# Kernel tuning notes

Hardware: AMD Instinct MI355X
Metric: run time of the kernel (lower is better)

The kernel has to match this reference:

```python
import jax, jax.numpy as jnp
import numpy as np

VOCAB = 50257  # nn.Embedding num_embeddings (vocab)
H = 128        # hidden_size
L = 20         # num_layers
T = 1024       # seq_len (time-major, batch_first=False)
B = 128        # batch


def setup_inputs() -> dict:
    key = jax.random.key(0)
    ks = jax.random.split(key, 6)
    s = 1.0 / np.sqrt(H)  # PyTorch LSTM init range
    return {
        "x": jax.random.randint(ks[0], (T, B), 0, VOCAB, dtype=jnp.int32),
        "emb": jax.random.normal(ks[1], (VOCAB, H), jnp.float32) * 0.02,
        "W_ih": jax.random.uniform(ks[2], (L, 4 * H, H), jnp.float32, -s, s),
        "W_hh": jax.random.uniform(ks[3], (L, 4 * H, H), jnp.float32, -s, s),
        "b_ih": jax.random.uniform(ks[4], (L, 4 * H), jnp.float32, -s, s),
        "b_hh": jax.random.uniform(ks[5], (L, 4 * H), jnp.float32, -s, s),
    }


def _lstm_layer(inp, Wih, Whh, b):
    # inp: [T, B, H]; PyTorch gate order: i, f, g, o
    h0 = jnp.zeros((inp.shape[1], H), inp.dtype)
    c0 = h0

    def step(carry, xt):
        h, c = carry
        pre = xt @ Wih.T + h @ Whh.T + b  # [B, 4H]
        i, f, g, o = jnp.split(pre, 4, axis=-1)
        c = jax.nn.sigmoid(f) * c + jax.nn.sigmoid(i) * jnp.tanh(g)
        h = jax.nn.sigmoid(o) * jnp.tanh(c)
        return (h, c), h

    _, hs = jax.lax.scan(step, (h0, c0), inp)
    return hs  # [T, B, H]


def reference(x, emb, W_ih, W_hh, b_ih, b_hh):
    embedded = emb[x]  # [T, B, H] embedding lookup
    out = embedded
    for l in range(L):  # stacked layers (structural loop, not a data dim)
        out = _lstm_layer(out, W_ih[l], W_hh[l], b_ih[l] + b_hh[l])
    return (out, embedded)
```

## Files before the change

kernel.cpp:

```cpp
#include <hip/hip_runtime.h>

#define T_ 1024
#define B_ 128
#define H_ 128
#define L_ 20
#define G4H_ 512
#define NCH 8
#define RING 64
#define GRP 4
#define FSTRIDE 32

typedef _Float16 f16x8 __attribute__((ext_vector_type(8)));
typedef _Float16 f16x4 __attribute__((ext_vector_type(4)));
typedef float f32x4 __attribute__((ext_vector_type(4)));

__device__ __forceinline__ float fast_sig(float x) {
  float e = __builtin_amdgcn_exp2f(-1.44269504f * x);
  return __builtin_amdgcn_rcpf(1.0f + e);
}
__device__ __forceinline__ float fast_tanh(float x) {
  float e = __builtin_amdgcn_exp2f(2.88539008f * x);
  return 1.0f - 2.0f * __builtin_amdgcn_rcpf(e + 1.0f);
}

__device__ __forceinline__ int flag_ld(const int* p) {
  int r;
  asm volatile("global_load_dword %0, %1, off sc1\n\ts_waitcnt vmcnt(0)"
               : "=v"(r) : "v"(p) : "memory");
  return r;
}
__device__ __forceinline__ void flag_st(int* p, int v) {
  asm volatile("global_store_dword %0, %1, off sc1" :: "v"(p), "v"(v) : "memory");
}
__device__ __forceinline__ void xld_sc1(f16x4* d, const _Float16* p) {
  asm volatile("global_load_dwordx2 %0, %1, off sc1" : "=&v"(*d) : "v"(p) : "memory");
}
__device__ __forceinline__ void xld_plain(f16x4* d, const _Float16* p) {
  asm volatile("global_load_dwordx2 %0, %1, off" : "=&v"(*d) : "v"(p) : "memory");
}
__device__ __forceinline__ void st32_sc1(_Float16* p, f16x8 a, f16x8 b) {
  asm volatile("global_store_dwordx4 %0, %1, off sc1\n\t"
               "global_store_dwordx4 %0, %2, off offset:16 sc1"
               :: "v"(p), "v"(a), "v"(b) : "memory");
}

__global__ void wconv_kernel(const float* __restrict__ Wih, const float* __restrict__ Whh,
                             _Float16* __restrict__ Wif, _Float16* __restrict__ Whf) {
  int i = blockIdx.x * 256 + threadIdx.x;
  if (i < L_ * G4H_ * H_) {
    Wif[i] = (_Float16)Wih[i];
    Whf[i] = (_Float16)Whh[i];
  }
}

__global__ void emb_kernel(const int* __restrict__ xids, const float* __restrict__ emb,
                           float* __restrict__ out_emb, _Float16* __restrict__ X0) {
  int row = blockIdx.x;
  int d = threadIdx.x;
  int tok = xids[row];
  float v = emb[(size_t)tok * H_ + d];
  out_emb[(size_t)row * H_ + d] = v;
  X0[(size_t)row * H_ + d] = (_Float16)v;
}

__launch_bounds__(512, 2)
__global__ void lstm_persist_kernel(const _Float16* __restrict__ Wif,
                                    const _Float16* __restrict__ Whf,
                                    const float* __restrict__ bih,
                                    const float* __restrict__ bhh,
                                    const _Float16* __restrict__ X0,
                                    _Float16* __restrict__ XR,
                                    float* __restrict__ out_h,
                                    int* __restrict__ rdy) {
  const int l = blockIdx.x >> 3;
  const int chunk = blockIdx.x & 7;
  const int lane = threadIdx.x & 63;
  const int wave = threadIdx.x >> 6;
  const int lr = lane & 15;
  const int lhi = lane >> 4;
  const int k0 = lhi * 8;
  const int ub = wave * 16;
  const int xrow = threadIdx.x >> 5;
  const int xseg = threadIdx.x & 31;

  f16x8 wi[4][4], wh[4][4];
  float bias[4];
  {
    const _Float16* wip = Wif + (size_t)l * G4H_ * H_;
    const _Float16* whp = Whf + (size_t)l * G4H_ * H_;
#pragma unroll
    for (int G = 0; G < 4; ++G) {
      int j = G * 128 + ub + lr;
      bias[G] = bih[l * G4H_ + j] + bhh[l * G4H_ + j];
#pragma unroll
      for (int kt = 0; kt < 4; ++kt) {
        wi[G][kt] = *(const f16x8*)(wip + (size_t)j * H_ + kt * 32 + k0);
        wh[G][kt] = *(const f16x8*)(whp + (size_t)j * H_ + kt * 32 + k0);
      }
    }
  }

  float cst[4] = {0.f, 0.f, 0.f, 0.f};
  f16x8 hf[4], xf[4];

  __shared__ _Float16 hstage[GRP][16][136];
  __shared__ _Float16 xstage[2][16][136];

  const size_t tile16 = (size_t)16 * H_;
  const _Float16* ring_in =
      (l > 0) ? XR + (size_t)((l - 1) * NCH + chunk) * RING * tile16 : X0;
  _Float16* ring_out = XR + (size_t)(l * NCH + chunk) * RING * tile16;

  int* rin = rdy + ((l - 1) * NCH + chunk) * FSTRIDE;
  int* rout = rdy + (l * NCH + chunk) * FSTRIDE;
  int* rcons = rdy + ((l + 1) * NCH + chunk) * FSTRIDE;

  auto xsrc = [&](int t) -> const _Float16* {
    return (l == 0) ? X0 + ((size_t)t * B_ + chunk * 16 + xrow) * H_ + xseg * 4
                    : ring_in + (size_t)(t & (RING - 1)) * tile16 + (size_t)xrow * H_ + xseg * 4;
  };

  int rin_cache = 0, rcons_cache = 0;

  for (int tg = 0; tg < T_; tg += GRP) {
    if (wave == 0) {
      if (l > 0 && rin_cache < tg + GRP) {
        int v;
        while ((v = flag_ld(rin)) < tg + GRP) __builtin_amdgcn_s_sleep(2);
        rin_cache = v;
      }
      if (l < L_ - 1) {
        int need = tg + 2 * GRP - RING;
        if (need > 0 && rcons_cache < need) {
          int v;
          while ((v = flag_ld(rcons)) < need) __builtin_amdgcn_s_sleep(2);
          rcons_cache = v;
        }
      }
    }
    __syncthreads();

    {
      f16x4 xs;
      const _Float16* sp = xsrc(tg);
      if (l == 0) xld_plain(&xs, sp); else xld_sc1(&xs, sp);
      asm volatile("s_waitcnt vmcnt(0)" ::: "memory");
      *(f16x4*)&xstage[0][xrow][xseg * 4] = xs;
    }
    asm volatile("s_waitcnt lgkmcnt(0)" ::: "memory");
    __builtin_amdgcn_s_barrier();

#pragma unroll
    for (int ti = 0; ti < GRP; ++ti) {
      const int t = tg + ti;

      if (t > 0) {
        const int ps = (ti + GRP - 1) & (GRP - 1);
#pragma unroll
        for (int kt = 0; kt < 4; ++kt)
          hf[kt] = *(const f16x8*)&hstage[ps][lr][kt * 32 + k0];
      } else {
#pragma unroll
        for (int kt = 0; kt < 4; ++kt)
#pragma unroll
          for (int i = 0; i < 8; ++i) hf[kt][i] = (_Float16)0.0f;
      }
#pragma unroll
      for (int kt = 0; kt < 4; ++kt)
        xf[kt] = *(const f16x8*)&xstage[t & 1][lr][kt * 32 + k0];

      f32x4 ai[4], ah[4];
#pragma unroll
      for (int G = 0; G < 4; ++G) {
        float bv = bias[G];
        ai[G][0] = bv; ai[G][1] = bv; ai[G][2] = bv; ai[G][3] = bv;
        ah[G][0] = 0.f; ah[G][1] = 0.f; ah[G][2] = 0.f; ah[G][3] = 0.f;
      }
#pragma unroll
      for (int kt = 0; kt < 4; ++kt)
#pragma unroll
        for (int G = 0; G < 4; ++G)
          ai[G] = __builtin_amdgcn_mfma_f32_16x16x32_f16(xf[kt], wi[G][kt], ai[G], 0, 0, 0);

      f16x4 xs;
      const bool pre = (ti + 1 < GRP);
      if (pre) {
        const _Float16* sp = xsrc(t + 1);
        if (l == 0) xld_plain(&xs, sp); else xld_sc1(&xs, sp);
      }

#pragma unroll
      for (int kt = 0; kt < 4; ++kt)
#pragma unroll
        for (int G = 0; G < 4; ++G)
          ah[G] = __builtin_amdgcn_mfma_f32_16x16x32_f16(hf[kt], wh[G][kt], ah[G], 0, 0, 0);

      float hnew[4];
#pragma unroll
      for (int r = 0; r < 4; ++r) {
        float pi = ai[0][r] + ah[0][r];
        float pf = ai[1][r] + ah[1][r];
        float pg = ai[2][r] + ah[2][r];
        float po = ai[3][r] + ah[3][r];
        float iv = fast_sig(pi);
        float fv = fast_sig(pf);
        float gv = fast_tanh(pg);
        float ov = fast_sig(po);
        float c = fv * cst[r] + iv * gv;
        cst[r] = c;
        hnew[r] = ov * fast_tanh(c);
      }

      if (l == L_ - 1) {
#pragma unroll
        for (int r = 0; r < 4; ++r)
          out_h[((size_t)t * B_ + chunk * 16 + lhi * 4 + r) * H_ + ub + lr] = hnew[r];
      }

      if (pre) {
        asm volatile("s_waitcnt vmcnt(0)" ::: "memory");
        *(f16x4*)&xstage[(t + 1) & 1][xrow][xseg * 4] = xs;
      }
#pragma unroll
      for (int r = 0; r < 4; ++r) hstage[ti][lhi * 4 + r][ub + lr] = (_Float16)hnew[r];

      asm volatile("s_waitcnt lgkmcnt(0)" ::: "memory");
      __builtin_amdgcn_s_barrier();
    }

    if (l < L_ - 1) {
      const int tid = threadIdx.x;
      const int ti2 = tid >> 7;
      const int rem = tid & 127;
      const int row = rem >> 3;
      const int seg = rem & 7;
      _Float16* dst = ring_out + (size_t)((tg + ti2) & (RING - 1)) * tile16 +
                      (size_t)row * H_ + seg * 16;
      const f16x8* src = (const f16x8*)&hstage[ti2][row][seg * 16];
      st32_sc1(dst, src[0], src[1]);
    }

    __syncthreads();
    if (threadIdx.x == 0) flag_st(rout, tg + GRP);
  }
}

extern "C" void kernel_launch(void* const* d_in, const int* in_sizes, int n_in,
                              void* d_out, int out_size, void* d_ws, size_t ws_size,
                              hipStream_t stream) {
  const int* xids = (const int*)d_in[0];
  const float* emb = (const float*)d_in[1];
  const float* Wih = (const float*)d_in[2];
  const float* Whh = (const float*)d_in[3];
  const float* bih = (const float*)d_in[4];
  const float* bhh = (const float*)d_in[5];
  float* out = (float*)d_out;
  float* out_h = out;
  float* out_emb = out + (size_t)T_ * B_ * H_;

  char* ws = (char*)d_ws;
  const size_t RDY_BYTES = (size_t)L_ * NCH * FSTRIDE * 4;
  const size_t X0_BYTES = (size_t)T_ * B_ * H_ * 2;
  const size_t XR_BYTES = (size_t)L_ * NCH * RING * 16 * H_ * 2;
  const size_t WF_BYTES = (size_t)L_ * G4H_ * H_ * 2;
  int* rdyp = (int*)ws;
  _Float16* X0 = (_Float16*)(ws + RDY_BYTES);
  _Float16* XR = (_Float16*)(ws + RDY_BYTES + X0_BYTES);
  _Float16* Wif = (_Float16*)(ws + RDY_BYTES + X0_BYTES + XR_BYTES);
  _Float16* Whf = (_Float16*)(ws + RDY_BYTES + X0_BYTES + XR_BYTES + WF_BYTES);

  hipMemsetAsync(rdyp, 0, RDY_BYTES, stream);
  wconv_kernel<<<(L_ * G4H_ * H_ + 255) / 256, 256, 0, stream>>>(Wih, Whh, Wif, Whf);
  emb_kernel<<<T_ * B_, H_, 0, stream>>>(xids, emb, out_emb, X0);

  void* args[] = {(void*)&Wif, (void*)&Whf, (void*)&bih, (void*)&bhh,
                  (void*)&X0,  (void*)&XR,  (void*)&out_h, (void*)&rdyp};
  hipLaunchCooperativeKernel((void*)lstm_persist_kernel, dim3(L_ * NCH), dim3(512),
                             args, 0, stream);
}
```

Before: 1.571 ms.

## Software-pipeline input projection one step ahead and deepen x prefetch ring

Restructures the per-timestep loop so the input-to-hidden MFMA for step t+1 is computed in the current step, off the recurrent critical path. The step-t+1 projection is seeded with the bias and accumulated directly with the hidden-state MFMAs, which drops the separate ah accumulators and the add. The x staging buffer grows from two to four slots, with loads issued three steps ahead and the upstream-layer wait target raised to cover the extra lookahead. This costs more registers for the second accumulator set and changes the flag and barrier schedule, including a flag wait before the loop.

New measurement: 1.568 ms. Within noise of the previous version (-0.2%).

```diff
diff --git a/kernel.cpp b/kernel.cpp
--- a/kernel.cpp
+++ b/kernel.cpp
@@ -101,10 +101,14 @@
   }
 
   float cst[4] = {0.f, 0.f, 0.f, 0.f};
-  f16x8 hf[4], xf[4];
+  f16x8 hf[4];
+#pragma unroll
+  for (int kt = 0; kt < 4; ++kt)
+#pragma unroll
+    for (int i = 0; i < 8; ++i) hf[kt][i] = (_Float16)0.0f;
 
   __shared__ _Float16 hstage[GRP][16][136];
-  __shared__ _Float16 xstage[2][16][136];
+  __shared__ _Float16 xstage[4][16][136];
 
   const size_t tile16 = (size_t)16 * H_;
   const _Float16* ring_in =
@@ -122,126 +126,158 @@
 
   int rin_cache = 0, rcons_cache = 0;
 
-  for (int tg = 0; tg < T_; tg += GRP) {
-    if (wave == 0) {
-      if (l > 0 && rin_cache < tg + GRP) {
-        int v;
-        while ((v = flag_ld(rin)) < tg + GRP) __builtin_amdgcn_s_sleep(2);
-        rin_cache = v;
-      }
-      if (l < L_ - 1) {
-        int need = tg + 2 * GRP - RING;
-        if (need > 0 && rcons_cache < need) {
-          int v;
-          while ((v = flag_ld(rcons)) < need) __builtin_amdgcn_s_sleep(2);
-          rcons_cache = v;
+  if (wave == 0 && l > 0) {
+    int tgt = 2 * GRP;
+    int v;
+    while ((v = flag_ld(rin)) < tgt) __builtin_amdgcn_s_sleep(2);
+    rin_cache = v;
+  }
+  __syncthreads();
+  {
+    f16x4 a0, a1, a2;
+    if (l == 0) { xld_plain(&a0, xsrc(0)); xld_plain(&a1, xsrc(1)); xld_plain(&a2, xsrc(2)); }
+    else        { xld_sc1(&a0, xsrc(0));   xld_sc1(&a1, xsrc(1));   xld_sc1(&a2, xsrc(2)); }
+    asm volatile("s_waitcnt vmcnt(0)" ::: "memory");
+    *(f16x4*)&xstage[0][xrow][xseg * 4] = a0;
+    *(f16x4*)&xstage[1][xrow][xseg * 4] = a1;
+    *(f16x4*)&xstage[2][xrow][xseg * 4] = a2;
+  }
+  asm volatile("s_waitcnt lgkmcnt(0)" ::: "memory");
+  __builtin_amdgcn_s_barrier();
+
+  f32x4 ai[4];
+  {
+    f16x8 xf0[4];
+#pragma unroll
+    for (int kt = 0; kt < 4; ++kt) xf0[kt] = *(const f16x8*)&xstage[0][lr][kt * 32 + k0];
+#pragma unroll
+    for (int G = 0; G < 4; ++G) {
+      float bv = bias[G];
+      ai[G][0] = bv; ai[G][1] = bv; ai[G][2] = bv; ai[G][3] = bv;
+    }
+#pragma unroll
+    for (int kt = 0; kt < 4; ++kt)
+#pragma unroll
+      for (int G = 0; G < 4; ++G)
+        ai[G] = __builtin_amdgcn_mfma_f32_16x16x32_f16(xf0[kt], wi[G][kt], ai[G], 0, 0, 0);
+  }
+
+  f16x4 xs;
+  bool xs_pending = false;
+
+  for (int t = 0; t < T_; ++t) {
+    if ((t & (GRP - 1)) == 0 && t > 0) {
+      const int tg = t;
+      if (wave == 0) {
+        if (l > 0) {
+          int tgt = tg + 2 * GRP; if (tgt > T_) tgt = T_;
+          if (rin_cache < tgt) {
+            int v;
+            while ((v = flag_ld(rin)) < tgt) __builtin_amdgcn_s_sleep(2);
+            rin_cache = v;
+          }
+        }
+        if (l < L_ - 1) {
+          int need = tg + 2 * GRP - RING;
+          if (need > 0 && rcons_cache < need) {
+            int v;
+            while ((v = flag_ld(rcons)) < need) __builtin_amdgcn_s_sleep(2);
+            rcons_cache = v;
+          }
         }
       }
-    }
-    __syncthreads();
-
-    {
-      f16x4 xs;
-      const _Float16* sp = xsrc(tg);
+      __builtin_amdgcn_s_barrier();
+    }
+
+    if (t > 0) {
+      const int ps = (t - 1) & (GRP - 1);
+#pragma unroll
+      for (int kt = 0; kt < 4; ++kt)
+        hf[kt] = *(const f16x8*)&hstage[ps][lr][kt * 32 + k0];
+    }
+
+#pragma unroll
+    for (int kt = 0; kt < 4; ++kt)
+#pragma unroll
+      for (int G = 0; G < 4; ++G)
+        ai[G] = __builtin_amdgcn_mfma_f32_16x16x32_f16(hf[kt], wh[G][kt], ai[G], 0, 0, 0);
+
+    const bool have_next = (t + 1 < T_);
+    f32x4 ain[4];
+    if (have_next) {
+      f16x8 xfn[4];
+#pragma unroll
+      for (int kt = 0; kt < 4; ++kt)
+        xfn[kt] = *(const f16x8*)&xstage[(t + 1) & 3][lr][kt * 32 + k0];
+#pragma unroll
+      for (int G = 0; G < 4; ++G) {
+        float bv = bias[G];
+        ain[G][0] = bv; ain[G][1] = bv; ain[G][2] = bv; ain[G][3] = bv;
+      }
+#pragma unroll
+      for (int kt = 0; kt < 4; ++kt)
+#pragma unroll
+        for (int G = 0; G < 4; ++G)
+          ain[G] = __builtin_amdgcn_mfma_f32_16x16x32_f16(xfn[kt], wi[G][kt], ain[G], 0, 0, 0);
+    }
+
+    if (xs_pending) {
+      asm volatile("s_waitcnt vmcnt(0)" ::: "memory");
+      *(f16x4*)&xstage[(t + 2) & 3][xrow][xseg * 4] = xs;
+    }
+    if (t + 3 < T_) {
+      const _Float16* sp = xsrc(t + 3);
       if (l == 0) xld_plain(&xs, sp); else xld_sc1(&xs, sp);
-      asm volatile("s_waitcnt vmcnt(0)" ::: "memory");
-      *(f16x4*)&xstage[0][xrow][xseg * 4] = xs;
-    }
+      xs_pending = true;
+    } else {
+      xs_pending = false;
+    }
+
+    float hnew[4];
+#pragma unroll
+    for (int r = 0; r < 4; ++r) {
+      float iv = fast_sig(ai[0][r]);
+      float fv = fast_sig(ai[1][r]);
+      float gv = fast_tanh(ai[2][r]);
+      float ov = fast_sig(ai[3][r]);
+      float c = fv * cst[r] + iv * gv;
+      cst[r] = c;
+      hnew[r] = ov * fast_tanh(c);
+    }
+
+    if (l == L_ - 1) {
+#pragma unroll
+      for (int r = 0; r < 4; ++r)
+        out_h[((size_t)t * B_ + chunk * 16 + lhi * 4 + r) * H_ + ub + lr] = hnew[r];
+    }
+
+#pragma unroll
+    for (int r = 0; r < 4; ++r) hstage[t & (GRP - 1)][lhi * 4 + r][ub + lr] = (_Float16)hnew[r];
+
+    if (have_next) {
+#pragma unroll
+      for (int G = 0; G < 4; ++G) ai[G] = ain[G];
+    }
+
     asm volatile("s_waitcnt lgkmcnt(0)" ::: "memory");
     __builtin_amdgcn_s_barrier();
 
-#pragma unroll
-    for (int ti = 0; ti < GRP; ++ti) {
-      const int t = tg + ti;
-
-      if (t > 0) {
-        const int ps = (ti + GRP - 1) & (GRP - 1);
-#pragma unroll
-        for (int kt = 0; kt < 4; ++kt)
-          hf[kt] = *(const f16x8*)&hstage[ps][lr][kt * 32 + k0];
-      } else {
-#pragma unroll
-        for (int kt = 0; kt < 4; ++kt)
-#pragma unroll
-          for (int i = 0; i < 8; ++i) hf[kt][i] = (_Float16)0.0f;
+    if ((t & (GRP - 1)) == GRP - 1) {
+      const int tg = t & ~(GRP - 1);
+      if (l < L_ - 1) {
+        const int tid = threadIdx.x;
+        const int ti2 = tid >> 7;
+        const int rem = tid & 127;
+        const int row = rem >> 3;
+        const int seg = rem & 7;
+        _Float16* dst = ring_out + (size_t)((tg + ti2) & (RING - 1)) * tile16 +
+                        (size_t)row * H_ + seg * 16;
+        const f16x8* src = (const f16x8*)&hstage[ti2][row][seg * 16];
+        st32_sc1(dst, src[0], src[1]);
       }
-#pragma unroll
-      for (int kt = 0; kt < 4; ++kt)
-        xf[kt] = *(const f16x8*)&xstage[t & 1][lr][kt * 32 + k0];
-
-      f32x4 ai[4], ah[4];
-#pragma unroll
-      for (int G = 0; G < 4; ++G) {
-        float bv = bias[G];
-        ai[G][0] = bv; ai[G][1] = bv; ai[G][2] = bv; ai[G][3] = bv;
-        ah[G][0] = 0.f; ah[G][1] = 0.f; ah[G][2] = 0.f; ah[G][3] = 0.f;
-      }
-#pragma unroll
-      for (int kt = 0; kt < 4; ++kt)
-#pragma unroll
-        for (int G = 0; G < 4; ++G)
-          ai[G] = __builtin_amdgcn_mfma_f32_16x16x32_f16(xf[kt], wi[G][kt], ai[G], 0, 0, 0);
-
-      f16x4 xs;
-      const bool pre = (ti + 1 < GRP);
-      if (pre) {
-        const _Float16* sp = xsrc(t + 1);
-        if (l == 0) xld_plain(&xs, sp); else xld_sc1(&xs, sp);
-      }
-
-#pragma unroll
-      for (int kt = 0; kt < 4; ++kt)
-#pragma unroll
-        for (int G = 0; G < 4; ++G)
-          ah[G] = __builtin_amdgcn_mfma_f32_16x16x32_f16(hf[kt], wh[G][kt], ah[G], 0, 0, 0);
-
-      float hnew[4];
-#pragma unroll
-      for (int r = 0; r < 4; ++r) {
-        float pi = ai[0][r] + ah[0][r];
-        float pf = ai[1][r] + ah[1][r];
-        float pg = ai[2][r] + ah[2][r];
-        float po = ai[3][r] + ah[3][r];
-        float iv = fast_sig(pi);
-        float fv = fast_sig(pf);
-        float gv = fast_tanh(pg);
-        float ov = fast_sig(po);
-        float c = fv * cst[r] + iv * gv;
-        cst[r] = c;
-        hnew[r] = ov * fast_tanh(c);
-      }
-
-      if (l == L_ - 1) {
-#pragma unroll
-        for (int r = 0; r < 4; ++r)
-          out_h[((size_t)t * B_ + chunk * 16 + lhi * 4 + r) * H_ + ub + lr] = hnew[r];
-      }
-
-      if (pre) {
-        asm volatile("s_waitcnt vmcnt(0)" ::: "memory");
-        *(f16x4*)&xstage[(t + 1) & 1][xrow][xseg * 4] = xs;
-      }
-#pragma unroll
-      for (int r = 0; r < 4; ++r) hstage[ti][lhi * 4 + r][ub + lr] = (_Float16)hnew[r];
-
-      asm volatile("s_waitcnt lgkmcnt(0)" ::: "memory");
-      __builtin_amdgcn_s_barrier();
-    }
-
-    if (l < L_ - 1) {
-      const int tid = threadIdx.x;
-      const int ti2 = tid >> 7;
-      const int rem = tid & 127;
-      const int row = rem >> 3;
-      const int seg = rem & 7;
-      _Float16* dst = ring_out + (size_t)((tg + ti2) & (RING - 1)) * tile16 +
-                      (size_t)row * H_ + seg * 16;
-      const f16x8* src = (const f16x8*)&hstage[ti2][row][seg * 16];
-      st32_sc1(dst, src[0], src[1]);
-    }
-
-    __syncthreads();
-    if (threadIdx.x == 0) flag_st(rout, tg + GRP);
+      __syncthreads();
+      if (threadIdx.x == 0) flag_st(rout, t + 1);
+    }
   }
 }
 
```

## Software-pipeline input projection one step ahead and defer ring stores

Applied to the files above, without the earlier changes.

Restructures the per-timestep loop so the input-projection MFMAs for step t+1 are computed while step t waits on the recurrent path, with ping-pong accumulators. X prefetch now runs four steps ahead into a 4-slot LDS buffer, and vmcnt waits are tuned per slot. The ring write-out and ready-flag publish for a group are deferred to the start of the next group, so their latency overlaps compute. The MFMA operands are swapped so each lane ends up with contiguous 4-wide outputs, which enables vectorized hstage, out_h and bias accesses. The cost is more complex synchronization, where a wrong vmcnt count or flag ordering could cause races.

New measurement: 1.511 ms. -3.9%, faster.

```diff
diff --git a/kernel.cpp b/kernel.cpp
--- a/kernel.cpp
+++ b/kernel.cpp
@@ -9,6 +9,7 @@
 #define RING 64
 #define GRP 4
 #define FSTRIDE 32
+#define STR 136
 
 typedef _Float16 f16x8 __attribute__((ext_vector_type(8)));
 typedef _Float16 f16x4 __attribute__((ext_vector_type(4)));
@@ -22,6 +23,9 @@
   float e = __builtin_amdgcn_exp2f(2.88539008f * x);
   return 1.0f - 2.0f * __builtin_amdgcn_rcpf(e + 1.0f);
 }
+
+#define VMW(n) asm volatile("s_waitcnt vmcnt(" #n ")" ::: "memory")
+#define LGKM0() asm volatile("s_waitcnt lgkmcnt(0)" ::: "memory")
 
 __device__ __forceinline__ int flag_ld(const int* p) {
   int r;
@@ -78,33 +82,34 @@
   const int wave = threadIdx.x >> 6;
   const int lr = lane & 15;
   const int lhi = lane >> 4;
-  const int k0 = lhi * 8;
   const int ub = wave * 16;
   const int xrow = threadIdx.x >> 5;
   const int xseg = threadIdx.x & 31;
 
   f16x8 wi[4][4], wh[4][4];
-  float bias[4];
+  f32x4 bias4[4];
   {
     const _Float16* wip = Wif + (size_t)l * G4H_ * H_;
     const _Float16* whp = Whf + (size_t)l * G4H_ * H_;
 #pragma unroll
     for (int G = 0; G < 4; ++G) {
       int j = G * 128 + ub + lr;
-      bias[G] = bih[l * G4H_ + j] + bhh[l * G4H_ + j];
 #pragma unroll
       for (int kt = 0; kt < 4; ++kt) {
-        wi[G][kt] = *(const f16x8*)(wip + (size_t)j * H_ + kt * 32 + k0);
-        wh[G][kt] = *(const f16x8*)(whp + (size_t)j * H_ + kt * 32 + k0);
+        wi[G][kt] = *(const f16x8*)(wip + (size_t)j * H_ + kt * 32 + lhi * 8);
+        wh[G][kt] = *(const f16x8*)(whp + (size_t)j * H_ + kt * 32 + lhi * 8);
       }
+      int jb = G * 128 + ub + lhi * 4;
+      bias4[G] = *(const f32x4*)&bih[l * G4H_ + jb];
+      bias4[G] += *(const f32x4*)&bhh[l * G4H_ + jb];
     }
   }
 
   float cst[4] = {0.f, 0.f, 0.f, 0.f};
-  f16x8 hf[4], xf[4];
-
-  __shared__ _Float16 hstage[GRP][16][136];
-  __shared__ _Float16 xstage[2][16][136];
+  f16x8 hf[4];
+
+  __shared__ _Float16 hstage[GRP][16][STR];
+  __shared__ _Float16 xstage[4][16][STR];
 
   const size_t tile16 = (size_t)16 * H_;
   const _Float16* ring_in =
@@ -122,127 +127,166 @@
 
   int rin_cache = 0, rcons_cache = 0;
 
+  if (wave == 0 && l > 0) {
+    int v;
+    while ((v = flag_ld(rin)) < 2 * GRP) __builtin_amdgcn_s_sleep(2);
+    rin_cache = v;
+  }
+  __syncthreads();
+  {
+    f16x4 a0, a1, a2, a3;
+    if (l == 0) { xld_plain(&a0, xsrc(0)); xld_plain(&a1, xsrc(1));
+                  xld_plain(&a2, xsrc(2)); xld_plain(&a3, xsrc(3)); }
+    else        { xld_sc1(&a0, xsrc(0)); xld_sc1(&a1, xsrc(1));
+                  xld_sc1(&a2, xsrc(2)); xld_sc1(&a3, xsrc(3)); }
+    VMW(0);
+    *(f16x4*)&xstage[0][xrow][xseg * 4] = a0;
+    *(f16x4*)&xstage[1][xrow][xseg * 4] = a1;
+    *(f16x4*)&xstage[2][xrow][xseg * 4] = a2;
+    *(f16x4*)&xstage[3][xrow][xseg * 4] = a3;
+  }
+  LGKM0();
+  __builtin_amdgcn_s_barrier();
+
+  f32x4 a0[4], a1[4];
+  {
+    f16x8 xf0[4];
+#pragma unroll
+    for (int kt = 0; kt < 4; ++kt)
+      xf0[kt] = *(const f16x8*)&xstage[0][lr][kt * 32 + lhi * 8];
+#pragma unroll
+    for (int G = 0; G < 4; ++G) a0[G] = bias4[G];
+#pragma unroll
+    for (int kt = 0; kt < 4; ++kt)
+#pragma unroll
+      for (int G = 0; G < 4; ++G)
+        a0[G] = __builtin_amdgcn_mfma_f32_16x16x32_f16(wi[G][kt], xf0[kt], a0[G], 0, 0, 0);
+  }
+
+  f16x4 xsp[2];
+
+#define STEP(ti, AC, AN)                                                         \
+  {                                                                              \
+    const int t = tg + (ti);                                                     \
+    if (t > 0) {                                                                 \
+      _Pragma("unroll")                                                          \
+      for (int kt = 0; kt < 4; ++kt)                                             \
+        hf[kt] = *(const f16x8*)&hstage[((ti) + 3) & 3][lr][kt * 32 + lhi * 8];  \
+      _Pragma("unroll")                                                          \
+      for (int kt = 0; kt < 4; ++kt)                                             \
+        _Pragma("unroll")                                                        \
+        for (int G = 0; G < 4; ++G)                                              \
+          AC[G] = __builtin_amdgcn_mfma_f32_16x16x32_f16(wh[G][kt], hf[kt], AC[G], 0, 0, 0); \
+    }                                                                            \
+    if (t + 1 < T_) {                                                            \
+      f16x8 xfn[4];                                                              \
+      _Pragma("unroll")                                                          \
+      for (int kt = 0; kt < 4; ++kt)                                             \
+        xfn[kt] = *(const f16x8*)&xstage[((ti) + 1) & 3][lr][kt * 32 + lhi * 8]; \
+      _Pragma("unroll")                                                          \
+      for (int G = 0; G < 4; ++G) AN[G] = bias4[G];                              \
+      _Pragma("unroll")                                                          \
+      for (int kt = 0; kt < 4; ++kt)                                             \
+        _Pragma("unroll")                                                        \
+        for (int G = 0; G < 4; ++G)                                              \
+          AN[G] = __builtin_amdgcn_mfma_f32_16x16x32_f16(wi[G][kt], xfn[kt], AN[G], 0, 0, 0); \
+    }                                                                            \
+    if (t >= 2 && t + 2 < T_) {              \
+      if (t >= T_ - 8) { VMW(0); }                                               \
+      else if ((ti) < 2) { VMW(3); }                                             \
+      else if (l == L_ - 1) { VMW(3); }                                          \
+      else { VMW(1); }                                                           \
+      *(f16x4*)&xstage[((ti) + 2) & 3][xrow][xseg * 4] = xsp[(ti) & 1];          \
+    }                                                                            \
+    if (t + 4 < T_) {           \
+      const _Float16* sp = xsrc(t + 4);                                          \
+      if (l == 0) xld_plain(&xsp[(ti) & 1], sp); else xld_sc1(&xsp[(ti) & 1], sp); \
+    }                                                                            \
+    float hnew[4];                                                               \
+    _Pragma("unroll")                                                            \
+    for (int r = 0; r < 4; ++r) {                                                \
+      float iv = fast_sig(AC[0][r]);                                             \
+      float fv = fast_sig(AC[1][r]);                                             \
+      float gv = fast_tanh(AC[2][r]);                                            \
+      float ov = fast_sig(AC[3][r]);                                             \
+      float c = fv * cst[r] + iv * gv;                                           \
+      cst[r] = c;                                                                \
+      hnew[r] = ov * fast_tanh(c);                                               \
+    }                                                                            \
+    {                                                                            \
+      f16x4 hp;                                                                  \
+      _Pragma("unroll")                                                          \
+      for (int r = 0; r < 4; ++r) hp[r] = (_Float16)hnew[r];                     \
+      *(f16x4*)&hstage[(ti)][lr][ub + lhi * 4] = hp;                             \
+    }                                                                            \
+    if (l == L_ - 1) {                                                           \
+      f32x4 ov4;                                                                 \
+      _Pragma("unroll")                                                          \
+      for (int r = 0; r < 4; ++r) ov4[r] = hnew[r];                              \
+      *(f32x4*)&out_h[((size_t)t * B_ + chunk * 16 + lr) * H_ + ub + lhi * 4] = ov4; \
+    }                                                                            \
+    LGKM0();                                                                     \
+    __builtin_amdgcn_s_barrier();                                                \
+  }
+
   for (int tg = 0; tg < T_; tg += GRP) {
-    if (wave == 0) {
-      if (l > 0 && rin_cache < tg + GRP) {
-        int v;
-        while ((v = flag_ld(rin)) < tg + GRP) __builtin_amdgcn_s_sleep(2);
-        rin_cache = v;
-      }
-      if (l < L_ - 1) {
-        int need = tg + 2 * GRP - RING;
-        if (need > 0 && rcons_cache < need) {
-          int v;
-          while ((v = flag_ld(rcons)) < need) __builtin_amdgcn_s_sleep(2);
-          rcons_cache = v;
+    if (tg > 0) {
+      if (wave == 0) {
+        if (l > 0) {
+          int tgt = tg + 2 * GRP; if (tgt > T_) tgt = T_;
+          if (rin_cache < tgt) {
+            int v;
+            while ((v = flag_ld(rin)) < tgt) __builtin_amdgcn_s_sleep(2);
+            rin_cache = v;
+          }
+        }
+        if (l < L_ - 1) {
+          int need = tg - 68;
+          if (need > 0 && rcons_cache < need) {
+            int v;
+            while ((v = flag_ld(rcons)) < need) __builtin_amdgcn_s_sleep(2);
+            rcons_cache = v;
+          }
         }
       }
-    }
-    __syncthreads();
-
-    {
-      f16x4 xs;
-      const _Float16* sp = xsrc(tg);
-      if (l == 0) xld_plain(&xs, sp); else xld_sc1(&xs, sp);
-      asm volatile("s_waitcnt vmcnt(0)" ::: "memory");
-      *(f16x4*)&xstage[0][xrow][xseg * 4] = xs;
-    }
-    asm volatile("s_waitcnt lgkmcnt(0)" ::: "memory");
-    __builtin_amdgcn_s_barrier();
-
-#pragma unroll
-    for (int ti = 0; ti < GRP; ++ti) {
-      const int t = tg + ti;
-
-      if (t > 0) {
-        const int ps = (ti + GRP - 1) & (GRP - 1);
-#pragma unroll
-        for (int kt = 0; kt < 4; ++kt)
-          hf[kt] = *(const f16x8*)&hstage[ps][lr][kt * 32 + k0];
-      } else {
-#pragma unroll
-        for (int kt = 0; kt < 4; ++kt)
-#pragma unroll
-          for (int i = 0; i < 8; ++i) hf[kt][i] = (_Float16)0.0f;
+      VMW(4);
+      __builtin_amdgcn_s_barrier();
+      if (threadIdx.x == 0) flag_st(rout, tg - GRP);
+      if (l < L_ - 1) {
+        const int tid = threadIdx.x;
+        const int ti2 = tid >> 7;
+        const int rem = tid & 127;
+        const int row = rem >> 3;
+        const int seg = rem & 7;
+        const f16x8 s0 = *(const f16x8*)&hstage[ti2][row][seg * 16];
+        const f16x8 s1 = *(const f16x8*)&hstage[ti2][row][seg * 16 + 8];
+        _Float16* dst = ring_out + (size_t)((tg - GRP + ti2) & (RING - 1)) * tile16 +
+                        (size_t)row * H_ + seg * 16;
+        st32_sc1(dst, s0, s1);
       }
-#pragma unroll
-      for (int kt = 0; kt < 4; ++kt)
-        xf[kt] = *(const f16x8*)&xstage[t & 1][lr][kt * 32 + k0];
-
-      f32x4 ai[4], ah[4];
-#pragma unroll
-      for (int G = 0; G < 4; ++G) {
-        float bv = bias[G];
-        ai[G][0] = bv; ai[G][1] = bv; ai[G][2] = bv; ai[G][3] = bv;
-        ah[G][0] = 0.f; ah[G][1] = 0.f; ah[G][2] = 0.f; ah[G][3] = 0.f;
-      }
-#pragma unroll
-      for (int kt = 0; kt < 4; ++kt)
-#pragma unroll
-        for (int G = 0; G < 4; ++G)
-          ai[G] = __builtin_amdgcn_mfma_f32_16x16x32_f16(xf[kt], wi[G][kt], ai[G], 0, 0, 0);
-
-      f16x4 xs;
-      const bool pre = (ti + 1 < GRP);
-      if (pre) {
-        const _Float16* sp = xsrc(t + 1);
-        if (l == 0) xld_plain(&xs, sp); else xld_sc1(&xs, sp);
-      }
-
-#pragma unroll
-      for (int kt = 0; kt < 4; ++kt)
-#pragma unroll
-        for (int G = 0; G < 4; ++G)
-          ah[G] = __builtin_amdgcn_mfma_f32_16x16x32_f16(hf[kt], wh[G][kt], ah[G], 0, 0, 0);
-
-      float hnew[4];
-#pragma unroll
-      for (int r = 0; r < 4; ++r) {
-        float pi = ai[0][r] + ah[0][r];
-        float pf = ai[1][r] + ah[1][r];
-        float pg = ai[2][r] + ah[2][r];
-        float po = ai[3][r] + ah[3][r];
-        float iv = fast_sig(pi);
-        float fv = fast_sig(pf);
-        float gv = fast_tanh(pg);
-        float ov = fast_sig(po);
-        float c = fv * cst[r] + iv * gv;
-        cst[r] = c;
-        hnew[r] = ov * fast_tanh(c);
-      }
-
-      if (l == L_ - 1) {
-#pragma unroll
-        for (int r = 0; r < 4; ++r)
-          out_h[((size_t)t * B_ + chunk * 16 + lhi * 4 + r) * H_ + ub + lr] = hnew[r];
-      }
-
-      if (pre) {
-        asm volatile("s_waitcnt vmcnt(0)" ::: "memory");
-        *(f16x4*)&xstage[(t + 1) & 1][xrow][xseg * 4] = xs;
-      }
-#pragma unroll
-      for (int r = 0; r < 4; ++r) hstage[ti][lhi * 4 + r][ub + lr] = (_Float16)hnew[r];
-
-      asm volatile("s_waitcnt lgkmcnt(0)" ::: "memory");
+      LGKM0();
       __builtin_amdgcn_s_barrier();
     }
-
-    if (l < L_ - 1) {
-      const int tid = threadIdx.x;
-      const int ti2 = tid >> 7;
-      const int rem = tid & 127;
-      const int row = rem >> 3;
-      const int seg = rem & 7;
-      _Float16* dst = ring_out + (size_t)((tg + ti2) & (RING - 1)) * tile16 +
-                      (size_t)row * H_ + seg * 16;
-      const f16x8* src = (const f16x8*)&hstage[ti2][row][seg * 16];
-      st32_sc1(dst, src[0], src[1]);
-    }
-
-    __syncthreads();
-    if (threadIdx.x == 0) flag_st(rout, tg + GRP);
-  }
+    STEP(0, a0, a1)
+    STEP(1, a1, a0)
+    STEP(2, a0, a1)
+    STEP(3, a1, a0)
+  }
+
+  if (l < L_ - 1) {
+    const int tid = threadIdx.x;
+    const int ti2 = tid >> 7;
+    const int rem = tid & 127;
+    const int row = rem >> 3;
+    const int seg = rem & 7;
+    const f16x8 s0 = *(const f16x8*)&hstage[ti2][row][seg * 16];
+    const f16x8 s1 = *(const f16x8*)&hstage[ti2][row][seg * 16 + 8];
+    _Float16* dst = ring_out + (size_t)((T_ - GRP + ti2) & (RING - 1)) * tile16 +
+                    (size_t)row * H_ + seg * 16;
+    st32_sc1(dst, s0, s1);
+  }
+  __syncthreads();
+  if (threadIdx.x == 0) flag_st(rout, T_);
 }
 
 extern "C" void kernel_launch(void* const* d_in, const int* in_sizes, int n_in,
```
